# Optimization experiments

Measured on AMD Instinct MI355X. Metric: run time of the kernel, lower is better.

## Reference

```python
import jax, jax.numpy as jnp
import numpy as np

N = 50000   # num_nodes
E = 640000  # num_edges (avg degree ~12.8)
D = 128     # input_dim
H = 128     # hidden_dim
T = 100     # targets per head


def setup_inputs() -> dict:
    key = jax.random.key(0)
    ks = jax.random.split(key, 20)
    w = lambda k, s: jax.random.normal(k, s, jnp.float32) * 0.02
    return {
        "x": jax.random.normal(ks[0], (N, D), jnp.float32),
        "edge_index": jax.random.randint(ks[1], (2, E), 0, N, dtype=jnp.int32),
        "edge_weight": jax.random.uniform(ks[2], (E,), jnp.float32),
        "ace_idx": jax.random.randint(ks[3], (T,), 0, N, dtype=jnp.int32),
        "h2_idx": jax.random.randint(ks[4], (T,), 0, N, dtype=jnp.int32),
        "W1": w(ks[5], (D, H)), "b1": jnp.zeros((H,), jnp.float32),
        "W2": w(ks[6], (H, H)), "b2": jnp.zeros((H,), jnp.float32),
        "W3": w(ks[7], (H, H)), "b3": jnp.zeros((H,), jnp.float32),
        "Wh": w(ks[8], (H, H)), "bh": jnp.zeros((H,), jnp.float32),
        "Wace": w(ks[9], (H, 1)), "bace": jnp.zeros((1,), jnp.float32),
        "Wh2": w(ks[10], (H, 1)), "bh2": jnp.zeros((1,), jnp.float32),
    }


def gcn_conv(x, src, dst, ew, W, b):
    # PyG GCNConv: add self-loops (weight 1), symmetric D^-1/2 (A+I) D^-1/2, then XW + b
    n = x.shape[0]
    xw = x @ W                                             # [N, H]
    deg = jax.ops.segment_sum(ew, dst, num_segments=n) + 1.0  # +1 from self-loop
    dinv = jax.lax.rsqrt(jnp.maximum(deg, 1e-12))          # deg >= 1 here
    norm = dinv[src] * ew * dinv[dst]                      # per-edge coefficient
    agg = jax.ops.segment_sum(norm[:, None] * xw[src], dst, num_segments=n)
    agg = agg + (dinv * dinv)[:, None] * xw                # self-loop contribution
    return agg + b


def reference(x, edge_index, edge_weight, ace_idx, h2_idx,
              W1, b1, W2, b2, W3, b3, Wh, bh, Wace, bace, Wh2, bh2):
    src, dst = edge_index[0], edge_index[1]
    h = jax.nn.relu(gcn_conv(x, src, dst, edge_weight, W1, b1))
    h = jax.nn.relu(gcn_conv(h, src, dst, edge_weight, W2, b2))
    h = jax.nn.relu(gcn_conv(h, src, dst, edge_weight, W3, b3))
    # dropout is identity in eval mode
    h = jax.nn.relu(h @ Wh + bh)
    ace_pred = h[ace_idx] @ Wace + bace   # [T, 1]
    h2_pred = h[h2_idx] @ Wh2 + bh2       # [T, 1]
    return jnp.concatenate([ace_pred, h2_pred], axis=0)  # [2T, 1]
```

## Files before the change

kernel.cpp:

```cpp
#include <hip/hip_runtime.h>
#include <math.h>

constexpr int N = 50000;
constexpr int E = 640000;
constexpr int D = 128;
constexpr int T = 100;
constexpr int MAXDEG = 64;
constexpr float SC = 256.0f;
constexpr float SCINV = 1.0f / 256.0f;
constexpr int GB = (N + 127) / 128;
constexpr int EBLK = (E + 255) / 256;
constexpr int ZTOT = N * 8 / 16;
constexpr int ZB = (ZTOT + 255) / 256;
constexpr int WCB = 3 * 16384 / 256;

typedef __attribute__((ext_vector_type(8))) _Float16 half8v;
typedef __attribute__((ext_vector_type(8))) unsigned short ushort8v;
typedef __attribute__((ext_vector_type(4))) float f32x4;

__device__ inline float dinv_of(unsigned int degY) {
  return 1.0f / sqrtf((float)degY * (1.0f / 16777216.0f) + 1.0f);
}


__global__ __launch_bounds__(256) void init_kernel(
    const float* __restrict__ W1, const float* __restrict__ W2,
    const float* __restrict__ W3, uint4* __restrict__ zero_v,
    unsigned short* __restrict__ wt0, unsigned short* __restrict__ wt1,
    unsigned short* __restrict__ w3kn) {
  int b = blockIdx.x, tid = threadIdx.x;
  if (b < ZB) {
    int i = b * 256 + tid;
    if (i < ZTOT) zero_v[i] = uint4{0, 0, 0, 0};
  } else {
    int idx = (b - ZB) * 256 + tid;
    int layer = idx >> 14;
    int r = idx & 16383;
    if (layer == 0) {
      int n = r >> 7, k = r & 127;
      _Float16 h = (_Float16)(W1[k * D + n] * SC);
      wt0[n * D + k] = *(unsigned short*)&h;
    } else if (layer == 1) {
      int n = r >> 7, k = r & 127;
      _Float16 h = (_Float16)W2[k * D + n];
      wt1[n * D + k] = *(unsigned short*)&h;
    } else {
      int k = r >> 7, n = r & 127;
      _Float16 h = (_Float16)W3[k * D + n];
      w3kn[k * D + n] = *(unsigned short*)&h;
    }
  }
}


__global__ __launch_bounds__(256) void fused_g1e_kernel(
    const float* __restrict__ x, const unsigned short* __restrict__ Bt,
    unsigned short* __restrict__ z1,
    const float* __restrict__ ew, const int* __restrict__ src,
    const int* __restrict__ dst,
    unsigned long long* __restrict__ degcnt, unsigned int* __restrict__ slot) {
  const int b = blockIdx.x;
  const int tid = threadIdx.x;
  if (b >= GB) {
    int e = (b - GB) * 256 + tid;
    if (e < E) {
      float w = ew[e];
      int d = dst[e];
      unsigned int fxdeg = __float2uint_rn(w * 16777216.0f);
      unsigned int fx16 = __float2uint_rn(w * 65536.0f);
      if (fx16 > 65535u) fx16 = 65535u;
      unsigned long long old = atomicAdd(&degcnt[d],
                                         ((unsigned long long)fxdeg << 32) | 1ull);
      unsigned int rank = (unsigned int)(old & 0xffffffffull);
      if (rank < MAXDEG)
        slot[(size_t)d * MAXDEG + rank] = (fx16 << 16) | (unsigned int)src[e];
    }
    return;
  }
  const int w = tid >> 6, lane = tid & 63;
  const int q = lane >> 4, n16 = lane & 15;
  const int rbase = w * 32;
  const int row0 = b * 128;
  size_t arow[2];
#pragma unroll
  for (int rt = 0; rt < 2; ++rt) {
    int gr = row0 + rbase + rt * 16 + n16;
    if (gr >= N) gr = N - 1;
    arow[rt] = (size_t)gr * D;
  }
  half8v a[4][2];
#pragma unroll
  for (int kc = 0; kc < 4; ++kc) {
    const int ko = kc * 32 + q * 8;
#pragma unroll
    for (int rt = 0; rt < 2; ++rt) {
      float4 v0 = *(const float4*)&x[arow[rt] + ko];
      float4 v1 = *(const float4*)&x[arow[rt] + ko + 4];
      half8v h;
      h[0] = (_Float16)v0.x; h[1] = (_Float16)v0.y;
      h[2] = (_Float16)v0.z; h[3] = (_Float16)v0.w;
      h[4] = (_Float16)v1.x; h[5] = (_Float16)v1.y;
      h[6] = (_Float16)v1.z; h[7] = (_Float16)v1.w;
      a[kc][rt] = h;
    }
  }
  f32x4 acc[2][8] = {};
#pragma unroll
  for (int kc = 0; kc < 4; ++kc) {
    const int ko = kc * 32 + q * 8;
#pragma unroll
    for (int ct = 0; ct < 8; ++ct) {
      int n = ct * 16 + n16;
      half8v bb = *(const half8v*)&Bt[n * D + ko];
#pragma unroll
      for (int rt = 0; rt < 2; ++rt) {
        acc[rt][ct] = __builtin_amdgcn_mfma_f32_16x16x32_f16(a[kc][rt], bb, acc[rt][ct], 0, 0, 0);
      }
    }
  }
#pragma unroll
  for (int rt = 0; rt < 2; ++rt) {
#pragma unroll
    for (int r = 0; r < 4; ++r) {
      int gr = row0 + rbase + rt * 16 + q * 4 + r;
      if (gr < N) {
#pragma unroll
        for (int ct = 0; ct < 8; ++ct) {
          int col = ct * 16 + n16;
          _Float16 h = (_Float16)acc[rt][ct][r];
          z1[(size_t)gr * D + col] = *(unsigned short*)&h;
        }
      }
    }
  }
}


__global__ __launch_bounds__(256) void gemm2_kernel(
    const unsigned short* __restrict__ A, const unsigned short* __restrict__ Bt,
    const uint2* __restrict__ degcnt, unsigned short* __restrict__ out) {
  const int tid = threadIdx.x;
  const int w = tid >> 6, lane = tid & 63;
  const int q = lane >> 4, n16 = lane & 15;
  const int rbase = w * 32;
  const int row0 = blockIdx.x * 128;

  size_t arow[2];
#pragma unroll
  for (int rt = 0; rt < 2; ++rt) {
    int gr = row0 + rbase + rt * 16 + n16;
    if (gr >= N) gr = N - 1;
    arow[rt] = (size_t)gr * D;
  }
  half8v a[4][2];
#pragma unroll
  for (int kc = 0; kc < 4; ++kc) {
    const int ko = kc * 32 + q * 8;
#pragma unroll
    for (int rt = 0; rt < 2; ++rt)
      a[kc][rt] = *(const half8v*)&A[arow[rt] + ko];
  }
  f32x4 acc[2][8] = {};
#pragma unroll
  for (int kc = 0; kc < 4; ++kc) {
    const int ko = kc * 32 + q * 8;
#pragma unroll
    for (int ct = 0; ct < 8; ++ct) {
      int n = ct * 16 + n16;
      half8v b = *(const half8v*)&Bt[n * D + ko];
#pragma unroll
      for (int rt = 0; rt < 2; ++rt) {
        acc[rt][ct] = __builtin_amdgcn_mfma_f32_16x16x32_f16(a[kc][rt], b, acc[rt][ct], 0, 0, 0);
      }
    }
  }
#pragma unroll
  for (int rt = 0; rt < 2; ++rt) {
#pragma unroll
    for (int r = 0; r < 4; ++r) {
      int gr = row0 + rbase + rt * 16 + q * 4 + r;
      if (gr < N) {
        float dv = dinv_of(degcnt[gr].y);
#pragma unroll
        for (int ct = 0; ct < 8; ++ct) {
          int col = ct * 16 + n16;
          _Float16 h = (_Float16)(acc[rt][ct][r] * dv);
          out[(size_t)gr * D + col] = *(unsigned short*)&h;
        }
      }
    }
  }
}


__global__ __launch_bounds__(256) void agg_kernel(
    const unsigned short* __restrict__ z, const unsigned int* __restrict__ slot,
    const uint2* __restrict__ degcnt, const float* __restrict__ bias,
    unsigned short* __restrict__ oP) {
  int g = (blockIdx.x * 256 + threadIdx.x) >> 4;
  int lane = threadIdx.x & 15;
  const unsigned int* degY = (const unsigned int*)degcnt;

  uint2 pg = degcnt[g];
  int cnt = (int)pg.x; if (cnt > MAXDEG) cnt = MAXDEG;
  float dvg = dinv_of(pg.y);
  half8v xv = *(const half8v*)&z[(size_t)g * D + lane * 8];
  float acc[8];
#pragma unroll
  for (int i = 0; i < 8; ++i) acc[i] = dvg * (float)xv[i];

  const unsigned int* sl = slot + (size_t)g * MAXDEG;
  int k = 0;
  for (; k + 8 <= cnt; k += 8) {
    uint4 pA = *(const uint4*)&sl[k];
    uint4 pB = *(const uint4*)&sl[k + 4];
    unsigned int s0 = pA.x & 0xffffu, s1 = pA.y & 0xffffu;
    unsigned int s2 = pA.z & 0xffffu, s3 = pA.w & 0xffffu;
    unsigned int s4 = pB.x & 0xffffu, s5 = pB.y & 0xffffu;
    unsigned int s6 = pB.z & 0xffffu, s7 = pB.w & 0xffffu;
    float c0 = (float)(pA.x >> 16) * (1.0f / 65536.0f) * dinv_of(degY[(s0 << 1) + 1]);
    float c1 = (float)(pA.y >> 16) * (1.0f / 65536.0f) * dinv_of(degY[(s1 << 1) + 1]);
    float c2 = (float)(pA.z >> 16) * (1.0f / 65536.0f) * dinv_of(degY[(s2 << 1) + 1]);
    float c3 = (float)(pA.w >> 16) * (1.0f / 65536.0f) * dinv_of(degY[(s3 << 1) + 1]);
    float c4 = (float)(pB.x >> 16) * (1.0f / 65536.0f) * dinv_of(degY[(s4 << 1) + 1]);
    float c5 = (float)(pB.y >> 16) * (1.0f / 65536.0f) * dinv_of(degY[(s5 << 1) + 1]);
    float c6 = (float)(pB.z >> 16) * (1.0f / 65536.0f) * dinv_of(degY[(s6 << 1) + 1]);
    float c7 = (float)(pB.w >> 16) * (1.0f / 65536.0f) * dinv_of(degY[(s7 << 1) + 1]);
    half8v v0 = *(const half8v*)&z[(size_t)s0 * D + lane * 8];
    half8v v1 = *(const half8v*)&z[(size_t)s1 * D + lane * 8];
    half8v v2 = *(const half8v*)&z[(size_t)s2 * D + lane * 8];
    half8v v3 = *(const half8v*)&z[(size_t)s3 * D + lane * 8];
    half8v v4 = *(const half8v*)&z[(size_t)s4 * D + lane * 8];
    half8v v5 = *(const half8v*)&z[(size_t)s5 * D + lane * 8];
    half8v v6 = *(const half8v*)&z[(size_t)s6 * D + lane * 8];
    half8v v7 = *(const half8v*)&z[(size_t)s7 * D + lane * 8];
#pragma unroll
    for (int i = 0; i < 8; ++i) {
      acc[i] = fmaf(c0, (float)v0[i], acc[i]);
      acc[i] = fmaf(c1, (float)v1[i], acc[i]);
      acc[i] = fmaf(c2, (float)v2[i], acc[i]);
      acc[i] = fmaf(c3, (float)v3[i], acc[i]);
      acc[i] = fmaf(c4, (float)v4[i], acc[i]);
      acc[i] = fmaf(c5, (float)v5[i], acc[i]);
      acc[i] = fmaf(c6, (float)v6[i], acc[i]);
      acc[i] = fmaf(c7, (float)v7[i], acc[i]);
    }
  }
  for (; k + 4 <= cnt; k += 4) {
    uint4 p = *(const uint4*)&sl[k];
    float c0 = (float)(p.x >> 16) * (1.0f / 65536.0f) * dinv_of(degY[(((p.x & 0xffffu)) << 1) + 1]);
    float c1 = (float)(p.y >> 16) * (1.0f / 65536.0f) * dinv_of(degY[(((p.y & 0xffffu)) << 1) + 1]);
    float c2 = (float)(p.z >> 16) * (1.0f / 65536.0f) * dinv_of(degY[(((p.z & 0xffffu)) << 1) + 1]);
    float c3 = (float)(p.w >> 16) * (1.0f / 65536.0f) * dinv_of(degY[(((p.w & 0xffffu)) << 1) + 1]);
    half8v v0 = *(const half8v*)&z[(size_t)(p.x & 0xffffu) * D + lane * 8];
    half8v v1 = *(const half8v*)&z[(size_t)(p.y & 0xffffu) * D + lane * 8];
    half8v v2 = *(const half8v*)&z[(size_t)(p.z & 0xffffu) * D + lane * 8];
    half8v v3 = *(const half8v*)&z[(size_t)(p.w & 0xffffu) * D + lane * 8];
#pragma unroll
    for (int i = 0; i < 8; ++i) {
      acc[i] = fmaf(c0, (float)v0[i], acc[i]);
      acc[i] = fmaf(c1, (float)v1[i], acc[i]);
      acc[i] = fmaf(c2, (float)v2[i], acc[i]);
      acc[i] = fmaf(c3, (float)v3[i], acc[i]);
    }
  }
  for (; k < cnt; ++k) {
    unsigned int p = sl[k];
    float dsv = dinv_of(degY[((p & 0xffffu) << 1) + 1]);
    float c = (float)(p >> 16) * (1.0f / 65536.0f) * dsv;
    half8v v = *(const half8v*)&z[(size_t)(p & 0xffffu) * D + lane * 8];
#pragma unroll
    for (int i = 0; i < 8; ++i) acc[i] = fmaf(c, (float)v[i], acc[i]);
  }

  half8v hv;
#pragma unroll
  for (int i = 0; i < 8; ++i)
    hv[i] = (_Float16)fmaxf(fmaf(dvg, acc[i], bias[lane * 8 + i] * SC), 0.f);
  *(half8v*)&oP[(size_t)g * D + lane * 8] = hv;
}


__global__ __launch_bounds__(256) void l23_part_kernel(
    const unsigned short* __restrict__ z2, const unsigned int* __restrict__ slot,
    const uint2* __restrict__ degcnt, const float* __restrict__ b2,
    const int* __restrict__ ace_idx, const int* __restrict__ h2_idx,
    float* __restrict__ pacc) {
  __shared__ float sacc[16][128];
  int b = blockIdx.x;
  int t = b >> 2, p = b & 3;
  int tid = threadIdx.x;
  int node = (t < T) ? ace_idx[t] : h2_idx[t - T];

  int grp = tid >> 4, lane = tid & 15;
  int G = p * 16 + grp;
  float b2l[8];
#pragma unroll
  for (int i = 0; i < 8; ++i) b2l[i] = b2[lane * 8 + i] * SC;

  uint2 pn = degcnt[node];
  int tcnt = (int)pn.x; if (tcnt > MAXDEG) tcnt = MAXDEG;
  const unsigned int* tsl = slot + (size_t)node * MAXDEG;
  int nitems = 1 + tcnt;
  float a[8] = {};
  for (int it = G; it < nitems; it += 64) {
    int u; float wgt;
    if (it == 0) { u = node; wgt = 1.0f; }
    else {
      unsigned int pk = tsl[it - 1];
      wgt = (float)(pk >> 16) * (1.0f / 65536.0f);
      u = (int)(pk & 0xffffu);
    }
    uint2 pu = degcnt[u];
    float dvu = dinv_of(pu.y);
    int cu = (int)pu.x; if (cu > MAXDEG) cu = MAXDEG;
    half8v xv = *(const half8v*)&z2[(size_t)u * D + lane * 8];
    float r[8];
#pragma unroll
    for (int i = 0; i < 8; ++i) r[i] = (float)xv[i];
    const unsigned int* usl = slot + (size_t)u * MAXDEG;
    int e = 0;
    for (; e + 8 <= cu; e += 8) {
      uint4 pA = *(const uint4*)&usl[e];
      uint4 pB = *(const uint4*)&usl[e + 4];
      float c0 = (float)(pA.x >> 16) * (1.0f / 65536.0f);
      float c1 = (float)(pA.y >> 16) * (1.0f / 65536.0f);
      float c2 = (float)(pA.z >> 16) * (1.0f / 65536.0f);
      float c3 = (float)(pA.w >> 16) * (1.0f / 65536.0f);
      float c4 = (float)(pB.x >> 16) * (1.0f / 65536.0f);
      float c5 = (float)(pB.y >> 16) * (1.0f / 65536.0f);
      float c6 = (float)(pB.z >> 16) * (1.0f / 65536.0f);
      float c7 = (float)(pB.w >> 16) * (1.0f / 65536.0f);
      half8v v0 = *(const half8v*)&z2[(size_t)(pA.x & 0xffffu) * D + lane * 8];
      half8v v1 = *(const half8v*)&z2[(size_t)(pA.y & 0xffffu) * D + lane * 8];
      half8v v2 = *(const half8v*)&z2[(size_t)(pA.z & 0xffffu) * D + lane * 8];
      half8v v3 = *(const half8v*)&z2[(size_t)(pA.w & 0xffffu) * D + lane * 8];
      half8v v4 = *(const half8v*)&z2[(size_t)(pB.x & 0xffffu) * D + lane * 8];
      half8v v5 = *(const half8v*)&z2[(size_t)(pB.y & 0xffffu) * D + lane * 8];
      half8v v6 = *(const half8v*)&z2[(size_t)(pB.z & 0xffffu) * D + lane * 8];
      half8v v7 = *(const half8v*)&z2[(size_t)(pB.w & 0xffffu) * D + lane * 8];
#pragma unroll
      for (int i = 0; i < 8; ++i) {
        r[i] = fmaf(c0, (float)v0[i], r[i]);
        r[i] = fmaf(c1, (float)v1[i], r[i]);
        r[i] = fmaf(c2, (float)v2[i], r[i]);
        r[i] = fmaf(c3, (float)v3[i], r[i]);
        r[i] = fmaf(c4, (float)v4[i], r[i]);
        r[i] = fmaf(c5, (float)v5[i], r[i]);
        r[i] = fmaf(c6, (float)v6[i], r[i]);
        r[i] = fmaf(c7, (float)v7[i], r[i]);
      }
    }
    for (; e + 4 <= cu; e += 4) {
      uint4 p4 = *(const uint4*)&usl[e];
      float c0 = (float)(p4.x >> 16) * (1.0f / 65536.0f);
      float c1 = (float)(p4.y >> 16) * (1.0f / 65536.0f);
      float c2 = (float)(p4.z >> 16) * (1.0f / 65536.0f);
      float c3 = (float)(p4.w >> 16) * (1.0f / 65536.0f);
      half8v v0 = *(const half8v*)&z2[(size_t)(p4.x & 0xffffu) * D + lane * 8];
      half8v v1 = *(const half8v*)&z2[(size_t)(p4.y & 0xffffu) * D + lane * 8];
      half8v v2 = *(const half8v*)&z2[(size_t)(p4.z & 0xffffu) * D + lane * 8];
      half8v v3 = *(const half8v*)&z2[(size_t)(p4.w & 0xffffu) * D + lane * 8];
#pragma unroll
      for (int i = 0; i < 8; ++i) {
        r[i] = fmaf(c0, (float)v0[i], r[i]);
        r[i] = fmaf(c1, (float)v1[i], r[i]);
        r[i] = fmaf(c2, (float)v2[i], r[i]);
        r[i] = fmaf(c3, (float)v3[i], r[i]);
      }
    }
    for (; e < cu; ++e) {
      unsigned int p2 = usl[e];
      float c2 = (float)(p2 >> 16) * (1.0f / 65536.0f);
      half8v v = *(const half8v*)&z2[(size_t)(p2 & 0xffffu) * D + lane * 8];
#pragma unroll
      for (int i = 0; i < 8; ++i) r[i] = fmaf(c2, (float)v[i], r[i]);
    }
#pragma unroll
    for (int i = 0; i < 8; ++i) {
      float h2 = fmaxf(fmaf(dvu, r[i], b2l[i]), 0.f);
      a[i] = fmaf(wgt, dvu * h2, a[i]);
    }
  }
#pragma unroll
  for (int i = 0; i < 8; ++i) sacc[grp][lane * 8 + i] = a[i];
  __syncthreads();

  if (tid < 128) {
    float s = 0.f;
#pragma unroll
    for (int gp = 0; gp < 16; ++gp) s += sacc[gp][tid];
    pacc[(size_t)(t * 4 + p) * 128 + tid] = s;
  }
}


__global__ __launch_bounds__(256) void l23_finish_kernel(
    const uint2* __restrict__ degcnt, const float* __restrict__ pacc,
    const float* __restrict__ b3, const unsigned short* __restrict__ w3kn,
    const float* __restrict__ Wh, const float* __restrict__ bh,
    const int* __restrict__ ace_idx, const int* __restrict__ h2_idx,
    const float* __restrict__ Wace, const float* __restrict__ bace,
    const float* __restrict__ Wh2, const float* __restrict__ bh2,
    float* __restrict__ out) {
  __shared__ unsigned short w3l[16384];
  __shared__ float svec[128];
  __shared__ float h3v[128];
  __shared__ float psum[2];
  int t = blockIdx.x;
  int tid = threadIdx.x;
  int node; const float* whead; float bhead;
  if (t < T) { node = ace_idx[t];     whead = Wace; bhead = bace[0]; }
  else       { node = h2_idx[t - T];  whead = Wh2;  bhead = bh2[0]; }

#pragma unroll
  for (int it = 0; it < 8; ++it) {
    int idx = tid + it * 256;
    *(ushort8v*)&w3l[idx * 8] = *(const ushort8v*)&w3kn[idx * 8];
  }
  if (tid < 128) {
    const float* pa = &pacc[(size_t)t * 4 * 128];
    float s = pa[tid] + pa[128 + tid] + pa[256 + tid] + pa[384 + tid];
    svec[tid] = s * dinv_of(degcnt[node].y);
  }
  __syncthreads();

  if (tid < 128) {
    float y = b3[tid] * SC;
#pragma unroll 16
    for (int k = 0; k < 128; ++k) {
      _Float16 wv = *(const _Float16*)&w3l[k * D + tid];
      y = fmaf(svec[k], (float)wv, y);
    }
    h3v[tid] = fmaxf(y, 0.f) * SCINV;
  }
  __syncthreads();

  float v = 0.f;
  if (tid < 128) {
    float acc = bh[tid];
#pragma unroll 16
    for (int k = 0; k < 128; ++k)
      acc = fmaf(h3v[k], Wh[k * D + tid], acc);
    v = fmaxf(acc, 0.f) * whead[tid];
  }
#pragma unroll
  for (int off = 32; off; off >>= 1) v += __shfl_down(v, off, 64);
  if (tid < 128 && (tid & 63) == 0) psum[tid >> 6] = v;
  __syncthreads();
  if (tid == 0) out[t] = psum[0] + psum[1] + bhead;
}


extern "C" void kernel_launch(void* const* d_in, const int* in_sizes, int n_in,
                              void* d_out, int out_size, void* d_ws, size_t ws_size,
                              hipStream_t stream) {
  const float* x    = (const float*)d_in[0];
  const int*   ei   = (const int*)d_in[1];
  const float* ew   = (const float*)d_in[2];
  const int*   ace  = (const int*)d_in[3];
  const int*   h2   = (const int*)d_in[4];
  const float* W1 = (const float*)d_in[5];  const float* b1 = (const float*)d_in[6];
  const float* W2 = (const float*)d_in[7];  const float* b2 = (const float*)d_in[8];
  const float* W3 = (const float*)d_in[9];  const float* b3 = (const float*)d_in[10];
  const float* Wh = (const float*)d_in[11]; const float* bh = (const float*)d_in[12];
  const float* Wace = (const float*)d_in[13]; const float* bace = (const float*)d_in[14];
  const float* Wh2  = (const float*)d_in[15]; const float* bh2  = (const float*)d_in[16];
  const int* src = ei;
  const int* dst = ei + E;

  char* w = (char*)d_ws;
  unsigned long long* degcnt = (unsigned long long*)w;  w += (size_t)N * 8;
  unsigned int* slot = (unsigned int*)w;     w += (size_t)N * MAXDEG * 4;
  unsigned short* wt0 = (unsigned short*)w;  w += 16384 * 2;
  unsigned short* wt1 = (unsigned short*)w;  w += 16384 * 2;
  unsigned short* w3kn = (unsigned short*)w; w += 16384 * 2;
  float* pacc = (float*)w;                   w += (size_t)2 * T * 4 * 128 * 4;
  unsigned short* zbuf = (unsigned short*)w; w += (size_t)N * D * 2;
  unsigned short* P1  = (unsigned short*)w;  w += (size_t)N * D * 2;

  const int AG = N * 16 / 256;

  init_kernel<<<ZB + WCB, 256, 0, stream>>>(W1, W2, W3, (uint4*)degcnt, wt0, wt1, w3kn);
  fused_g1e_kernel<<<GB + EBLK, 256, 0, stream>>>(x, wt0, zbuf, ew, src, dst, degcnt, slot);
  agg_kernel<<<AG, 256, 0, stream>>>(zbuf, slot, (const uint2*)degcnt, b1, P1);
  gemm2_kernel<<<GB, 256, 0, stream>>>(P1, wt1, (const uint2*)degcnt, zbuf);
  l23_part_kernel<<<4 * 2 * T, 256, 0, stream>>>(zbuf, slot, (const uint2*)degcnt,
                                                 b2, ace, h2, pacc);
  l23_finish_kernel<<<2 * T, 256, 0, stream>>>((const uint2*)degcnt, pacc, b3, w3kn,
                                               Wh, bh, ace, h2,
                                               Wace, bace, Wh2, bh2, (float*)d_out);
}
```

Measured before the change: 210.9 us.

## Replace 64-bit degree atomics with 32-bit counts and precomputed dinv array

The edge pass now does a 32-bit count atomic instead of a 64-bit packed count+weighted-degree atomic. A new degpass kernel sums the quantized 16-bit weights from the slot lists and writes a per-node float dinv array. Downstream kernels then read dinv directly rather than recomputing rsqrt from gathered degree words. The cost is an extra kernel launch and a pass over the slot array. Degree precision also drops from 24-bit to 16-bit fixed-point weights, which changes numerics slightly.

```diff
diff --git a/kernel.cpp b/kernel.cpp
--- a/kernel.cpp
+++ b/kernel.cpp
@@ -10,17 +10,13 @@
 constexpr float SCINV = 1.0f / 256.0f;
 constexpr int GB = (N + 127) / 128;
 constexpr int EBLK = (E + 255) / 256;
-constexpr int ZTOT = N * 8 / 16;
+constexpr int ZTOT = N * 4 / 16;
 constexpr int ZB = (ZTOT + 255) / 256;
 constexpr int WCB = 3 * 16384 / 256;
 
 typedef __attribute__((ext_vector_type(8))) _Float16 half8v;
 typedef __attribute__((ext_vector_type(8))) unsigned short ushort8v;
 typedef __attribute__((ext_vector_type(4))) float f32x4;
-
-__device__ inline float dinv_of(unsigned int degY) {
-  return 1.0f / sqrtf((float)degY * (1.0f / 16777216.0f) + 1.0f);
-}
 
 
 __global__ __launch_bounds__(256) void init_kernel(
@@ -58,7 +54,7 @@
     unsigned short* __restrict__ z1,
     const float* __restrict__ ew, const int* __restrict__ src,
     const int* __restrict__ dst,
-    unsigned long long* __restrict__ degcnt, unsigned int* __restrict__ slot) {
+    unsigned int* __restrict__ cnt32, unsigned int* __restrict__ slot) {
   const int b = blockIdx.x;
   const int tid = threadIdx.x;
   if (b >= GB) {
@@ -66,12 +62,9 @@
     if (e < E) {
       float w = ew[e];
       int d = dst[e];
-      unsigned int fxdeg = __float2uint_rn(w * 16777216.0f);
       unsigned int fx16 = __float2uint_rn(w * 65536.0f);
       if (fx16 > 65535u) fx16 = 65535u;
-      unsigned long long old = atomicAdd(&degcnt[d],
-                                         ((unsigned long long)fxdeg << 32) | 1ull);
-      unsigned int rank = (unsigned int)(old & 0xffffffffull);
+      unsigned int rank = atomicAdd(&cnt32[d], 1u);
       if (rank < MAXDEG)
         slot[(size_t)d * MAXDEG + rank] = (fx16 << 16) | (unsigned int)src[e];
     }
@@ -136,9 +129,25 @@
 }
 
 
+__global__ __launch_bounds__(256) void degpass_kernel(
+    const unsigned int* __restrict__ slot, const unsigned int* __restrict__ cnt32,
+    float* __restrict__ dinvA) {
+  int g = (blockIdx.x * 256 + threadIdx.x) >> 4;
+  int lane = threadIdx.x & 15;
+  int cnt = (int)cnt32[g]; if (cnt > MAXDEG) cnt = MAXDEG;
+  const unsigned int* sl = slot + (size_t)g * MAXDEG;
+  unsigned int s = 0;
+  for (int k = lane; k < cnt; k += 16) s += (sl[k] >> 16);
+#pragma unroll
+  for (int off = 8; off; off >>= 1) s += __shfl_xor(s, off, 16);
+  if (lane == 0)
+    dinvA[g] = 1.0f / sqrtf((float)s * (1.0f / 65536.0f) + 1.0f);
+}
+
+
 __global__ __launch_bounds__(256) void gemm2_kernel(
     const unsigned short* __restrict__ A, const unsigned short* __restrict__ Bt,
-    const uint2* __restrict__ degcnt, unsigned short* __restrict__ out) {
+    const float* __restrict__ dinvA, unsigned short* __restrict__ out) {
   const int tid = threadIdx.x;
   const int w = tid >> 6, lane = tid & 63;
   const int q = lane >> 4, n16 = lane & 15;
@@ -180,7 +189,7 @@
     for (int r = 0; r < 4; ++r) {
       int gr = row0 + rbase + rt * 16 + q * 4 + r;
       if (gr < N) {
-        float dv = dinv_of(degcnt[gr].y);
+        float dv = dinvA[gr];
 #pragma unroll
         for (int ct = 0; ct < 8; ++ct) {
           int col = ct * 16 + n16;
@@ -195,15 +204,13 @@
 
 __global__ __launch_bounds__(256) void agg_kernel(
     const unsigned short* __restrict__ z, const unsigned int* __restrict__ slot,
-    const uint2* __restrict__ degcnt, const float* __restrict__ bias,
-    unsigned short* __restrict__ oP) {
+    const unsigned int* __restrict__ cnt32, const float* __restrict__ dinvA,
+    const float* __restrict__ bias, unsigned short* __restrict__ oP) {
   int g = (blockIdx.x * 256 + threadIdx.x) >> 4;
   int lane = threadIdx.x & 15;
-  const unsigned int* degY = (const unsigned int*)degcnt;
-
-  uint2 pg = degcnt[g];
-  int cnt = (int)pg.x; if (cnt > MAXDEG) cnt = MAXDEG;
-  float dvg = dinv_of(pg.y);
+
+  int cnt = (int)cnt32[g]; if (cnt > MAXDEG) cnt = MAXDEG;
+  float dvg = dinvA[g];
   half8v xv = *(const half8v*)&z[(size_t)g * D + lane * 8];
   float acc[8];
 #pragma unroll
@@ -218,14 +225,14 @@
     unsigned int s2 = pA.z & 0xffffu, s3 = pA.w & 0xffffu;
     unsigned int s4 = pB.x & 0xffffu, s5 = pB.y & 0xffffu;
     unsigned int s6 = pB.z & 0xffffu, s7 = pB.w & 0xffffu;
-    float c0 = (float)(pA.x >> 16) * (1.0f / 65536.0f) * dinv_of(degY[(s0 << 1) + 1]);
-    float c1 = (float)(pA.y >> 16) * (1.0f / 65536.0f) * dinv_of(degY[(s1 << 1) + 1]);
-    float c2 = (float)(pA.z >> 16) * (1.0f / 65536.0f) * dinv_of(degY[(s2 << 1) + 1]);
-    float c3 = (float)(pA.w >> 16) * (1.0f / 65536.0f) * dinv_of(degY[(s3 << 1) + 1]);
-    float c4 = (float)(pB.x >> 16) * (1.0f / 65536.0f) * dinv_of(degY[(s4 << 1) + 1]);
-    float c5 = (float)(pB.y >> 16) * (1.0f / 65536.0f) * dinv_of(degY[(s5 << 1) + 1]);
-    float c6 = (float)(pB.z >> 16) * (1.0f / 65536.0f) * dinv_of(degY[(s6 << 1) + 1]);
-    float c7 = (float)(pB.w >> 16) * (1.0f / 65536.0f) * dinv_of(degY[(s7 << 1) + 1]);
+    float c0 = (float)(pA.x >> 16) * (1.0f / 65536.0f) * dinvA[s0];
+    float c1 = (float)(pA.y >> 16) * (1.0f / 65536.0f) * dinvA[s1];
+    float c2 = (float)(pA.z >> 16) * (1.0f / 65536.0f) * dinvA[s2];
+    float c3 = (float)(pA.w >> 16) * (1.0f / 65536.0f) * dinvA[s3];
+    float c4 = (float)(pB.x >> 16) * (1.0f / 65536.0f) * dinvA[s4];
+    float c5 = (float)(pB.y >> 16) * (1.0f / 65536.0f) * dinvA[s5];
+    float c6 = (float)(pB.z >> 16) * (1.0f / 65536.0f) * dinvA[s6];
+    float c7 = (float)(pB.w >> 16) * (1.0f / 65536.0f) * dinvA[s7];
     half8v v0 = *(const half8v*)&z[(size_t)s0 * D + lane * 8];
     half8v v1 = *(const half8v*)&z[(size_t)s1 * D + lane * 8];
     half8v v2 = *(const half8v*)&z[(size_t)s2 * D + lane * 8];
@@ -248,10 +255,10 @@
   }
   for (; k + 4 <= cnt; k += 4) {
     uint4 p = *(const uint4*)&sl[k];
-    float c0 = (float)(p.x >> 16) * (1.0f / 65536.0f) * dinv_of(degY[(((p.x & 0xffffu)) << 1) + 1]);
-    float c1 = (float)(p.y >> 16) * (1.0f / 65536.0f) * dinv_of(degY[(((p.y & 0xffffu)) << 1) + 1]);
-    float c2 = (float)(p.z >> 16) * (1.0f / 65536.0f) * dinv_of(degY[(((p.z & 0xffffu)) << 1) + 1]);
-    float c3 = (float)(p.w >> 16) * (1.0f / 65536.0f) * dinv_of(degY[(((p.w & 0xffffu)) << 1) + 1]);
+    float c0 = (float)(p.x >> 16) * (1.0f / 65536.0f) * dinvA[p.x & 0xffffu];
+    float c1 = (float)(p.y >> 16) * (1.0f / 65536.0f) * dinvA[p.y & 0xffffu];
+    float c2 = (float)(p.z >> 16) * (1.0f / 65536.0f) * dinvA[p.z & 0xffffu];
+    float c3 = (float)(p.w >> 16) * (1.0f / 65536.0f) * dinvA[p.w & 0xffffu];
     half8v v0 = *(const half8v*)&z[(size_t)(p.x & 0xffffu) * D + lane * 8];
     half8v v1 = *(const half8v*)&z[(size_t)(p.y & 0xffffu) * D + lane * 8];
     half8v v2 = *(const half8v*)&z[(size_t)(p.z & 0xffffu) * D + lane * 8];
@@ -266,8 +273,7 @@
   }
   for (; k < cnt; ++k) {
     unsigned int p = sl[k];
-    float dsv = dinv_of(degY[((p & 0xffffu) << 1) + 1]);
-    float c = (float)(p >> 16) * (1.0f / 65536.0f) * dsv;
+    float c = (float)(p >> 16) * (1.0f / 65536.0f) * dinvA[p & 0xffffu];
     half8v v = *(const half8v*)&z[(size_t)(p & 0xffffu) * D + lane * 8];
 #pragma unroll
     for (int i = 0; i < 8; ++i) acc[i] = fmaf(c, (float)v[i], acc[i]);
@@ -283,7 +289,8 @@
 
 __global__ __launch_bounds__(256) void l23_part_kernel(
     const unsigned short* __restrict__ z2, const unsigned int* __restrict__ slot,
-    const uint2* __restrict__ degcnt, const float* __restrict__ b2,
+    const unsigned int* __restrict__ cnt32, const float* __restrict__ dinvA,
+    const float* __restrict__ b2,
     const int* __restrict__ ace_idx, const int* __restrict__ h2_idx,
     float* __restrict__ pacc) {
   __shared__ float sacc[16][128];
@@ -298,8 +305,7 @@
 #pragma unroll
   for (int i = 0; i < 8; ++i) b2l[i] = b2[lane * 8 + i] * SC;
 
-  uint2 pn = degcnt[node];
-  int tcnt = (int)pn.x; if (tcnt > MAXDEG) tcnt = MAXDEG;
+  int tcnt = (int)cnt32[node]; if (tcnt > MAXDEG) tcnt = MAXDEG;
   const unsigned int* tsl = slot + (size_t)node * MAXDEG;
   int nitems = 1 + tcnt;
   float a[8] = {};
@@ -311,9 +317,8 @@
       wgt = (float)(pk >> 16) * (1.0f / 65536.0f);
       u = (int)(pk & 0xffffu);
     }
-    uint2 pu = degcnt[u];
-    float dvu = dinv_of(pu.y);
-    int cu = (int)pu.x; if (cu > MAXDEG) cu = MAXDEG;
+    float dvu = dinvA[u];
+    int cu = (int)cnt32[u]; if (cu > MAXDEG) cu = MAXDEG;
     half8v xv = *(const half8v*)&z2[(size_t)u * D + lane * 8];
     float r[8];
 #pragma unroll
@@ -396,7 +401,7 @@
 
 
 __global__ __launch_bounds__(256) void l23_finish_kernel(
-    const uint2* __restrict__ degcnt, const float* __restrict__ pacc,
+    const float* __restrict__ dinvA, const float* __restrict__ pacc,
     const float* __restrict__ b3, const unsigned short* __restrict__ w3kn,
     const float* __restrict__ Wh, const float* __restrict__ bh,
     const int* __restrict__ ace_idx, const int* __restrict__ h2_idx,
@@ -421,7 +426,7 @@
   if (tid < 128) {
     const float* pa = &pacc[(size_t)t * 4 * 128];
     float s = pa[tid] + pa[128 + tid] + pa[256 + tid] + pa[384 + tid];
-    svec[tid] = s * dinv_of(degcnt[node].y);
+    svec[tid] = s * dinvA[node];
   }
   __syncthreads();
 
@@ -470,7 +475,8 @@
   const int* dst = ei + E;
 
   char* w = (char*)d_ws;
-  unsigned long long* degcnt = (unsigned long long*)w;  w += (size_t)N * 8;
+  unsigned int* cnt32 = (unsigned int*)w;    w += (size_t)N * 4;
+  float* dinvA = (float*)w;                  w += (size_t)N * 4;
   unsigned int* slot = (unsigned int*)w;     w += (size_t)N * MAXDEG * 4;
   unsigned short* wt0 = (unsigned short*)w;  w += 16384 * 2;
   unsigned short* wt1 = (unsigned short*)w;  w += 16384 * 2;
@@ -481,13 +487,14 @@
 
   const int AG = N * 16 / 256;
 
-  init_kernel<<<ZB + WCB, 256, 0, stream>>>(W1, W2, W3, (uint4*)degcnt, wt0, wt1, w3kn);
-  fused_g1e_kernel<<<GB + EBLK, 256, 0, stream>>>(x, wt0, zbuf, ew, src, dst, degcnt, slot);
-  agg_kernel<<<AG, 256, 0, stream>>>(zbuf, slot, (const uint2*)degcnt, b1, P1);
-  gemm2_kernel<<<GB, 256, 0, stream>>>(P1, wt1, (const uint2*)degcnt, zbuf);
-  l23_part_kernel<<<4 * 2 * T, 256, 0, stream>>>(zbuf, slot, (const uint2*)degcnt,
+  init_kernel<<<ZB + WCB, 256, 0, stream>>>(W1, W2, W3, (uint4*)cnt32, wt0, wt1, w3kn);
+  fused_g1e_kernel<<<GB + EBLK, 256, 0, stream>>>(x, wt0, zbuf, ew, src, dst, cnt32, slot);
+  degpass_kernel<<<AG, 256, 0, stream>>>(slot, cnt32, dinvA);
+  agg_kernel<<<AG, 256, 0, stream>>>(zbuf, slot, cnt32, dinvA, b1, P1);
+  gemm2_kernel<<<GB, 256, 0, stream>>>(P1, wt1, dinvA, zbuf);
+  l23_part_kernel<<<4 * 2 * T, 256, 0, stream>>>(zbuf, slot, cnt32, dinvA,
                                                  b2, ace, h2, pacc);
-  l23_finish_kernel<<<2 * T, 256, 0, stream>>>((const uint2*)degcnt, pacc, b3, w3kn,
+  l23_finish_kernel<<<2 * T, 256, 0, stream>>>(dinvA, pacc, b3, w3kn,
                                                Wh, bh, ace, h2,
                                                Wace, bace, Wh2, bh2, (float*)d_out);
 }
```

Result: no change. 209.1 us (-0.8%).
